# Performance work log

Measured on AMD Instinct MI355X. Metric: run time of the kernel, lower is better.

The kernel has to match this reference:

```python
import jax, jax.numpy as jnp
import numpy as np

LP, LQ, B, IN, HID = 256, 256, 32, 512, 512
H = 2 * HID          # internal hidden size (hidden_size * 2)
IN2 = 2 * IN         # Up/Uq feature dim after self-concat
IN4 = 4 * IN


def setup_inputs() -> dict:
    key = jax.random.key(0)
    ks = jax.random.split(key, 12)
    def w(k, shape, fan):
        return (jax.random.normal(k, shape, jnp.float32) / np.float32(np.sqrt(fan)))
    return {
        "up": jax.random.normal(ks[0], (LP, B, IN), jnp.float32),
        "uq": jax.random.normal(ks[1], (LQ, B, IN), jnp.float32),
        "v0": jax.random.normal(ks[2], (B, H), jnp.float32),    # torch.randn v
        "Vvec": jax.random.normal(ks[3], (B, H), jnp.float32),  # torch.randn V (squeezed)
        "Wp": w(ks[4], (H, IN2), IN2),
        "Wq": w(ks[5], (H, IN2), IN2),
        "Wv": w(ks[6], (H, H), H),
        "Wg": w(ks[7], (IN4, IN4), IN4),
        "W_ih": w(ks[8], (3 * H, IN2), IN2),
        "W_hh": w(ks[9], (3 * H, H), H),
        "b_ih": w(ks[10], (3 * H,), H),
        "b_hh": w(ks[11], (3 * H,), H),
    }


def reference(up, uq, v0, Vvec, Wp, Wq, Wv, Wg, W_ih, W_hh, b_ih, b_hh):
    in2 = 2 * up.shape[2]
    # mixer indices are arange -> Up/Uq are just feature self-concats
    Up = jnp.concatenate([up, up], axis=2)   # [lp, B, in2]
    Uq = jnp.concatenate([uq, uq], axis=2)   # [lq, B, in2]
    # hoist loop-invariant projections (original recomputes Wq(Uq) each step)
    WUp = jnp.einsum('pbi,hi->pbh', Up, Wp)  # [lp, B, H]
    WUq = jnp.einsum('qbi,hi->qbh', Uq, Wq)  # [lq, B, H]

    def gru_cell(x, h):
        gi = x @ W_ih.T + b_ih
        gh = h @ W_hh.T + b_hh
        i_r, i_z, i_n = jnp.split(gi, 3, axis=1)
        h_r, h_z, h_n = jnp.split(gh, 3, axis=1)
        r = jax.nn.sigmoid(i_r + h_r)
        z = jax.nn.sigmoid(i_z + h_z)
        n = jnp.tanh(i_n + r * h_n)
        return (1.0 - z) * n + z * h

    def step(v, xs):
        up_i, wup_i = xs                                   # [B,in2], [B,H]
        x = jnp.tanh(wup_i[None] + WUq + (v @ Wv.T)[None])  # [lq, B, H]
        s = jnp.einsum('qbh,bh->bq', x, Vvec)               # [B, lq]
        a = jax.nn.softmax(s, axis=1)
        c = jnp.einsum('bq,qbd->bd', a, Uq)                 # [B, in2]
        r = jnp.concatenate([up_i, c], axis=1)              # [B, in4]
        g = jax.nn.sigmoid(r @ Wg.T)
        c_ = (g * r)[:, in2:]                               # gated context half
        v_new = gru_cell(c_, v)
        return v_new, v_new

    _, vs = jax.lax.scan(step, v0, (Up, WUp))   # vs: [lp, B, H]
    # dropout in eval mode = identity
    return vs
```

## Files before the change

### kernel.cpp

```cpp
#include <hip/hip_runtime.h>


#define NB 32
#define WOFF 16384

__device__ __forceinline__ float fsig(float x) { return 1.0f / (1.0f + __expf(-x)); }
__device__ __forceinline__ float ftanh(float x) { return 1.0f - 2.0f / (1.0f + __expf(2.0f * x)); }

__device__ __forceinline__ float wred(float a) {
#pragma unroll
  for (int o = 32; o >= 1; o >>= 1) a += __shfl_xor(a, o, 64);
  return a;
}

__device__ __forceinline__ float cload(const float* p) {
  return __hip_atomic_load(p, __ATOMIC_RELAXED, __HIP_MEMORY_SCOPE_AGENT);
}
__device__ __forceinline__ void cstore(float* p, float v) {
  __hip_atomic_store(p, v, __ATOMIC_RELAXED, __HIP_MEMORY_SCOPE_AGENT);
}
__device__ __forceinline__ int cloadi(const int* p) {
  return __hip_atomic_load(p, __ATOMIC_RELAXED, __HIP_MEMORY_SCOPE_AGENT);
}

__device__ __forceinline__ void bgbar(int* sub, int* root, int bar) {
  __syncthreads();
  if (threadIdx.x == 0) {
    int old = __hip_atomic_fetch_add(sub, 1, __ATOMIC_RELAXED, __HIP_MEMORY_SCOPE_AGENT);
    if (old == 16 * bar - 1)
      __hip_atomic_fetch_add(root, 1, __ATOMIC_RELAXED, __HIP_MEMORY_SCOPE_AGENT);
    int tgt = 4 * bar, spins = 0;
    for (;;) {
      if (cloadi(root) >= tgt) break;
      __builtin_amdgcn_s_sleep(2);
      if (((++spins) & 255) == 0 &&
          __hip_atomic_load(root, __ATOMIC_ACQUIRE, __HIP_MEMORY_SCOPE_AGENT) >= tgt)
        break;
    }
  }
  __syncthreads();
}

__global__ __launch_bounds__(256) void k_init(
    const float* __restrict__ v0, const float* __restrict__ Wp,
    const float* __restrict__ Wg, float* __restrict__ wsbase,
    float* __restrict__ vbuf, float* __restrict__ Wpf, float* __restrict__ Wg2f) {
  int i = blockIdx.x * 256 + threadIdx.x;
  if (i < WOFF) ((int*)wsbase)[i] = 0;
  if (i < NB * 1024) vbuf[i] = v0[i];
  if (i < 1024 * 512) {
    int n = i >> 9, k = i & 511;
    Wpf[i] = Wp[(size_t)n * 1024 + k] + Wp[(size_t)n * 1024 + k + 512];
  }
  if (i < 1024 * 1024) {
    int j = i >> 10, kk = i & 1023;
    const float* wr = Wg + (size_t)(1024 + j) * 2048;
    Wg2f[i] = (kk < 512) ? (wr[kk] + wr[kk + 512]) : (wr[kk + 512] + wr[kk + 1024]);
  }
}

__global__ __launch_bounds__(256) void k_wuq(
    const float* __restrict__ A, const float* __restrict__ Wq, float* __restrict__ C) {
  __shared__ float As[16][65];
  __shared__ float Bs[16][65];
  int bm = blockIdx.x * 64, bn = blockIdx.y * 64;
  int t = threadIdx.x;
  int tx = t & 15, ty = t >> 4;
  float acc[4][4] = {};
  for (int k0 = 0; k0 < 512; k0 += 16) {
#pragma unroll
    for (int l = 0; l < 4; ++l) {
      int idx = t + l * 256;
      int row = idx >> 4, kk = idx & 15;
      As[kk][row] = A[(size_t)(bm + row) * 512 + k0 + kk];
      Bs[kk][row] = Wq[(size_t)(bn + row) * 1024 + k0 + kk] +
                    Wq[(size_t)(bn + row) * 1024 + k0 + kk + 512];
    }
    __syncthreads();
#pragma unroll
    for (int kk = 0; kk < 16; ++kk) {
      float a0[4], b0[4];
#pragma unroll
      for (int i = 0; i < 4; ++i) a0[i] = As[kk][ty * 4 + i];
#pragma unroll
      for (int j = 0; j < 4; ++j) b0[j] = Bs[kk][tx * 4 + j];
#pragma unroll
      for (int i = 0; i < 4; ++i)
#pragma unroll
        for (int j = 0; j < 4; ++j) acc[i][j] += a0[i] * b0[j];
    }
    __syncthreads();
  }
#pragma unroll
  for (int i = 0; i < 4; ++i)
#pragma unroll
    for (int j = 0; j < 4; ++j)
      C[(size_t)(bm + ty * 4 + i) * 1024 + bn + tx * 4 + j] = acc[i][j];
}

__global__ __launch_bounds__(512, 2) void k_loop(
    const float* __restrict__ up, const float* __restrict__ uq,
    const float* __restrict__ Vvec, const float* __restrict__ Wv,
    const float* __restrict__ W_hh, const float* __restrict__ b_hh,
    const float* __restrict__ W_ih, const float* __restrict__ b_ih,
    float* __restrict__ out, float* __restrict__ ws) {
  int* cbase = (int*)ws;

  float* vbuf  = ws + WOFF;
  float* tbuf  = ws + WOFF + 32768;
  float* ghbuf = ws + WOFF + 65536;
  float* sbuf  = ws + WOFF + 163840;
  float* chalf = ws + WOFF + 172032;
  float* cbuf  = ws + WOFF + 188416;
  float* Wpf   = ws + WOFF + 221184;
  float* Wg2f  = ws + WOFF + 745472;
  float* WUq   = ws + WOFF + 1794048;

  int bid = blockIdx.x;
  int tid = threadIdx.x, lane = tid & 63, wave = tid >> 6;

  __shared__ float smem[12288];

  int s = bid & 63, bg = bid >> 6, b0 = bg * 8;
  bool is_t = (s < 16);
  int b3 = b0 + (s >> 3), i0 = (s & 7) * 64;

  int* subc = cbase + (bg * 8 + (s >> 4)) * 64;
  int* rootc = cbase + (bg * 8 + 4) * 64;

  float vvreg[16];
#pragma unroll
  for (int i = 0; i < 16; ++i)
    vvreg[i] = Vvec[(size_t)(b0 + wave) * 1024 + lane + i * 64];

  int ho5 = tid >> 3, bb5 = tid & 7;
  int h5 = s * 16 + ho5, b5 = b0 + bb5;
  float vloc = 0.0f;
  if (tid < 128) vloc = cload(vbuf + (size_t)b5 * 1024 + h5);

  int bar = 0;

  for (int p = 0; p < 256; ++p) {
    {
      float tmp[16];
#pragma unroll
      for (int i = 0; i < 16; ++i)
        tmp[i] = cload(vbuf + (size_t)b0 * 1024 + tid + i * 512);
#pragma unroll
      for (int i = 0; i < 16; ++i) smem[tid + i * 512] = tmp[i];
      if (is_t) {
        float tu[8];
#pragma unroll
        for (int i = 0; i < 8; ++i)
          tu[i] = up[((size_t)p * NB + b0) * 512 + tid + i * 512];
#pragma unroll
        for (int i = 0; i < 8; ++i) smem[8192 + tid + i * 512] = tu[i];
      }
      __syncthreads();
      float vreg[8][16];
#pragma unroll
      for (int bb = 0; bb < 8; ++bb)
#pragma unroll
        for (int i = 0; i < 16; ++i)
          vreg[bb][i] = smem[bb * 1024 + lane + i * 64];
      int n0 = s * 64 + wave * 8;
      for (int rr = 0; rr < 8; ++rr) {
        int n = n0 + rr;
        float acc[8];
#pragma unroll
        for (int bb = 0; bb < 8; ++bb) acc[bb] = 0.0f;
        if (is_t) {
          const float* wr = Wv + (size_t)n * 1024;
#pragma unroll
          for (int i = 0; i < 16; ++i) {
            float w = wr[lane + i * 64];
#pragma unroll
            for (int bb = 0; bb < 8; ++bb) acc[bb] = fmaf(w, vreg[bb][i], acc[bb]);
          }
          const float* wp = Wpf + (size_t)n * 512;
#pragma unroll
          for (int i = 0; i < 8; ++i) {
            float w = wp[lane + i * 64];
#pragma unroll
            for (int bb = 0; bb < 8; ++bb)
              acc[bb] = fmaf(w, smem[8192 + bb * 512 + lane + i * 64], acc[bb]);
          }
#pragma unroll
          for (int bb = 0; bb < 8; ++bb) {
            float a = wred(acc[bb]);
            if (lane == 0) cstore(tbuf + (size_t)(b0 + bb) * 1024 + n, a);
          }
        } else {
          int m = n - 1024;
          const float* wr = W_hh + (size_t)m * 1024;
#pragma unroll
          for (int i = 0; i < 16; ++i) {
            float w = wr[lane + i * 64];
#pragma unroll
            for (int bb = 0; bb < 8; ++bb) acc[bb] = fmaf(w, vreg[bb][i], acc[bb]);
          }
          float bias = b_hh[m];
#pragma unroll
          for (int bb = 0; bb < 8; ++bb) {
            float a = wred(acc[bb]);
            if (lane == 0) cstore(ghbuf + (size_t)(b0 + bb) * 3072 + m, a + bias);
          }
        }
      }
    }
    ++bar; bgbar(subc, rootc, bar);

    {
      float tmp[16];
#pragma unroll
      for (int i = 0; i < 16; ++i)
        tmp[i] = cload(tbuf + (size_t)b0 * 1024 + tid + i * 512);
#pragma unroll
      for (int i = 0; i < 16; ++i) smem[tid + i * 512] = tmp[i];
      __syncthreads();
      float treg[16];
#pragma unroll
      for (int i = 0; i < 16; ++i) treg[i] = smem[wave * 1024 + lane + i * 64];
      int bq = b0 + wave;
      for (int qq = 0; qq < 4; ++qq) {
        int q = s * 4 + qq;
        const float* wu = WUq + ((size_t)q * NB + bq) * 1024;
        float a = 0.0f;
#pragma unroll
        for (int i = 0; i < 16; ++i)
          a += ftanh(treg[i] + __builtin_nontemporal_load(wu + lane + i * 64)) * vvreg[i];
        a = wred(a);
        if (lane == 0) cstore(sbuf + bq * 256 + q, a);
      }
    }
    ++bar; bgbar(subc, rootc, bar);

    {
      float* a_s  = smem;
      float* red  = smem + 256;
      float* part = smem + 512;
      int b = b3;
      float sv = -1e30f;
      if (tid < 256) sv = cload(sbuf + b * 256 + tid);
      float m = sv;
#pragma unroll
      for (int o = 32; o >= 1; o >>= 1) m = fmaxf(m, __shfl_xor(m, o, 64));
      if (lane == 0 && wave < 4) red[wave] = m;
      __syncthreads();
      float bm = fmaxf(fmaxf(red[0], red[1]), fmaxf(red[2], red[3]));
      __syncthreads();
      float e = 0.0f;
      if (tid < 256) e = __expf(sv - bm);
      float se = e;
#pragma unroll
      for (int o = 32; o >= 1; o >>= 1) se += __shfl_xor(se, o, 64);
      if (lane == 0 && wave < 4) red[wave] = se;
      __syncthreads();
      float tot = red[0] + red[1] + red[2] + red[3];
      if (tid < 256) a_s[tid] = e / tot;
      __syncthreads();
      float acc = 0.0f;
      for (int qq = 0; qq < 32; ++qq) {
        int q = wave * 32 + qq;
        acc += a_s[q] *
               __builtin_nontemporal_load(uq + ((size_t)q * NB + b) * 512 + i0 + lane);
      }
      part[wave * 64 + lane] = acc;
      __syncthreads();
      if (tid < 64) {
        float c = 0.0f;
#pragma unroll
        for (int w = 0; w < 8; ++w) c += part[w * 64 + tid];
        cstore(chalf + (size_t)b * 512 + i0 + tid, c);
      }
    }
    ++bar; bgbar(subc, rootc, bar);

    {
      float tc[8];
#pragma unroll
      for (int i = 0; i < 8; ++i)
        tc[i] = cload(chalf + (size_t)b0 * 512 + tid + i * 512);
#pragma unroll
      for (int i = 0; i < 8; ++i) smem[tid + i * 512] = tc[i];
      __syncthreads();
      float rreg[8][16];
#pragma unroll
      for (int bb = 0; bb < 8; ++bb) {
#pragma unroll
        for (int i = 0; i < 8; ++i)
          rreg[bb][i] = up[((size_t)p * NB + b0 + bb) * 512 + lane + i * 64];
#pragma unroll
        for (int i = 0; i < 8; ++i)
          rreg[bb][8 + i] = smem[bb * 512 + lane + i * 64];
      }
      int j0 = s * 16 + wave * 2;
      for (int rr = 0; rr < 2; ++rr) {
        int j = j0 + rr;
        const float* wr = Wg2f + (size_t)j * 1024;
        float acc[8];
#pragma unroll
        for (int bb = 0; bb < 8; ++bb) acc[bb] = 0.0f;
#pragma unroll
        for (int i = 0; i < 16; ++i) {
          float w = wr[lane + i * 64];
#pragma unroll
          for (int bb = 0; bb < 8; ++bb) acc[bb] = fmaf(w, rreg[bb][i], acc[bb]);
        }
#pragma unroll
        for (int bb = 0; bb < 8; ++bb) {
          float a = wred(acc[bb]);
          if (lane == 0) {
            float cv = smem[bb * 512 + (j & 511)];
            cstore(cbuf + (size_t)(b0 + bb) * 1024 + j, fsig(a) * cv);
          }
        }
      }
    }
    ++bar; bgbar(subc, rootc, bar);

    {
      float ghr = 0.0f, ghz = 0.0f, ghn = 0.0f;
      if (tid < 128) {
        const float* ghb = ghbuf + (size_t)b5 * 3072;
        ghr = cload(ghb + h5);
        ghz = cload(ghb + 1024 + h5);
        ghn = cload(ghb + 2048 + h5);
      }
      float tmp[16];
#pragma unroll
      for (int i = 0; i < 16; ++i)
        tmp[i] = cload(cbuf + (size_t)b0 * 1024 + tid + i * 512);
#pragma unroll
      for (int i = 0; i < 16; ++i) smem[tid + i * 512] = tmp[i];
      __syncthreads();
      float creg[8][16];
#pragma unroll
      for (int bb = 0; bb < 8; ++bb)
#pragma unroll
        for (int i = 0; i < 16; ++i)
          creg[bb][i] = smem[bb * 1024 + lane + i * 64];
      float* gi_s = smem + 8192;
      for (int k = 0; k < 6; ++k) {
        int idx = wave * 6 + k;
        int g = idx >> 4, ho = idx & 15;
        int r = g * 1024 + s * 16 + ho;
        const float* wr = W_ih + (size_t)r * 1024;
        float acc[8];
#pragma unroll
        for (int bb = 0; bb < 8; ++bb) acc[bb] = 0.0f;
#pragma unroll
        for (int i = 0; i < 16; ++i) {
          float w = wr[lane + i * 64];
#pragma unroll
          for (int bb = 0; bb < 8; ++bb) acc[bb] = fmaf(w, creg[bb][i], acc[bb]);
        }
        float bias = b_ih[r];
#pragma unroll
        for (int bb = 0; bb < 8; ++bb) {
          float a = wred(acc[bb]);
          if (lane == 0) gi_s[idx * 8 + bb] = a + bias;
        }
      }
      __syncthreads();
      if (tid < 128) {
        float gir = gi_s[(0 * 16 + ho5) * 8 + bb5];
        float giz = gi_s[(1 * 16 + ho5) * 8 + bb5];
        float gin = gi_s[(2 * 16 + ho5) * 8 + bb5];
        float rg = fsig(gir + ghr);
        float z  = fsig(giz + ghz);
        float nn = ftanh(gin + rg * ghn);
        float vn = (1.0f - z) * nn + z * vloc;
        vloc = vn;
        cstore(vbuf + (size_t)b5 * 1024 + h5, vn);
        __builtin_nontemporal_store(vn, out + ((size_t)p * NB + b5) * 1024 + h5);
      }
    }
    ++bar; bgbar(subc, rootc, bar);
  }
}

extern "C" void kernel_launch(void* const* d_in, const int* in_sizes, int n_in,
                              void* d_out, int out_size, void* d_ws, size_t ws_size,
                              hipStream_t stream) {
  const float* up = (const float*)d_in[0];
  const float* uq = (const float*)d_in[1];
  const float* v0 = (const float*)d_in[2];
  const float* Vvec = (const float*)d_in[3];
  const float* Wp = (const float*)d_in[4];
  const float* Wq = (const float*)d_in[5];
  const float* Wv = (const float*)d_in[6];
  const float* Wg = (const float*)d_in[7];
  const float* W_ih = (const float*)d_in[8];
  const float* W_hh = (const float*)d_in[9];
  const float* b_ih = (const float*)d_in[10];
  const float* b_hh = (const float*)d_in[11];
  float* out = (float*)d_out;
  float* ws = (float*)d_ws;

  float* vbuf = ws + WOFF;
  float* Wpf  = ws + WOFF + 221184;
  float* Wg2f = ws + WOFF + 745472;
  float* WUq  = ws + WOFF + 1794048;

  k_init<<<4096, 256, 0, stream>>>(v0, Wp, Wg, ws, vbuf, Wpf, Wg2f);
  k_wuq<<<dim3(128, 16), 256, 0, stream>>>(uq, Wq, WUq);
  k_loop<<<256, 512, 0, stream>>>(up, uq, Vvec, Wv, W_hh, b_hh, W_ih, b_ih, out, ws);
}
```

Before: 32.34 ms.

## Prefetch per-phase weights and inputs into registers before grid barriers

Loads for the next phase (WUq rows, uq context rows, Wg rows, the first two W_ih rows and the gh gate values) are issued into registers before each grid-wide barrier instead of after it. Their memory latency can then overlap the barrier wait in this persistent, barrier-heavy recurrent kernel. The prefetch loops are fully unrolled and the data stays in registers. The cost is higher VGPR pressure across barriers, which could cause spills or lower occupancy.

```diff
diff --git a/kernel.cpp b/kernel.cpp
--- a/kernel.cpp
+++ b/kernel.cpp
@@ -208,6 +208,16 @@
         }
       }
     }
+    float wuq_pf[4][16];
+    {
+      int bq = b0 + wave;
+#pragma unroll
+      for (int qq = 0; qq < 4; ++qq) {
+        const float* wu = WUq + ((size_t)(s * 4 + qq) * NB + bq) * 1024;
+#pragma unroll
+        for (int i = 0; i < 16; ++i) wuq_pf[qq][i] = wu[lane + i * 64];
+      }
+    }
     ++bar; bgbar(subc, rootc, bar);
 
     {
@@ -222,17 +232,21 @@
 #pragma unroll
       for (int i = 0; i < 16; ++i) treg[i] = smem[wave * 1024 + lane + i * 64];
       int bq = b0 + wave;
+#pragma unroll
       for (int qq = 0; qq < 4; ++qq) {
         int q = s * 4 + qq;
-        const float* wu = WUq + ((size_t)q * NB + bq) * 1024;
         float a = 0.0f;
 #pragma unroll
         for (int i = 0; i < 16; ++i)
-          a += ftanh(treg[i] + __builtin_nontemporal_load(wu + lane + i * 64)) * vvreg[i];
+          a += ftanh(treg[i] + wuq_pf[qq][i]) * vvreg[i];
         a = wred(a);
         if (lane == 0) cstore(sbuf + bq * 256 + q, a);
       }
     }
+    float uq_pf[32];
+#pragma unroll
+    for (int qq = 0; qq < 32; ++qq)
+      uq_pf[qq] = uq[((size_t)(wave * 32 + qq) * NB + b3) * 512 + i0 + lane];
     ++bar; bgbar(subc, rootc, bar);
 
     {
@@ -260,11 +274,9 @@
       if (tid < 256) a_s[tid] = e / tot;
       __syncthreads();
       float acc = 0.0f;
-      for (int qq = 0; qq < 32; ++qq) {
-        int q = wave * 32 + qq;
-        acc += a_s[q] *
-               __builtin_nontemporal_load(uq + ((size_t)q * NB + b) * 512 + i0 + lane);
-      }
+#pragma unroll
+      for (int qq = 0; qq < 32; ++qq)
+        acc += a_s[wave * 32 + qq] * uq_pf[qq];
       part[wave * 64 + lane] = acc;
       __syncthreads();
       if (tid < 64) {
@@ -274,6 +286,16 @@
         cstore(chalf + (size_t)b * 512 + i0 + tid, c);
       }
     }
+    float wg_pf[2][16];
+    {
+      int j0 = s * 16 + wave * 2;
+#pragma unroll
+      for (int rr = 0; rr < 2; ++rr) {
+        const float* wr = Wg2f + (size_t)(j0 + rr) * 1024;
+#pragma unroll
+        for (int i = 0; i < 16; ++i) wg_pf[rr][i] = wr[lane + i * 64];
+      }
+    }
     ++bar; bgbar(subc, rootc, bar);
 
     {
@@ -295,15 +317,15 @@
           rreg[bb][8 + i] = smem[bb * 512 + lane + i * 64];
       }
       int j0 = s * 16 + wave * 2;
+#pragma unroll
       for (int rr = 0; rr < 2; ++rr) {
         int j = j0 + rr;
-        const float* wr = Wg2f + (size_t)j * 1024;
         float acc[8];
 #pragma unroll
         for (int bb = 0; bb < 8; ++bb) acc[bb] = 0.0f;
 #pragma unroll
         for (int i = 0; i < 16; ++i) {
-          float w = wr[lane + i * 64];
+          float w = wg_pf[rr][i];
 #pragma unroll
           for (int bb = 0; bb < 8; ++bb) acc[bb] = fmaf(w, rreg[bb][i], acc[bb]);
         }
@@ -317,16 +339,25 @@
         }
       }
     }
+    float wih_pf[2][16];
+#pragma unroll
+    for (int k = 0; k < 2; ++k) {
+      int idx = wave * 6 + k;
+      int r = (idx >> 4) * 1024 + s * 16 + (idx & 15);
+      const float* wr = W_ih + (size_t)r * 1024;
+#pragma unroll
+      for (int i = 0; i < 16; ++i) wih_pf[k][i] = wr[lane + i * 64];
+    }
+    float ghr = 0.0f, ghz = 0.0f, ghn = 0.0f;
+    if (tid < 128) {
+      const float* ghb = ghbuf + (size_t)b5 * 3072;
+      ghr = cload(ghb + h5);
+      ghz = cload(ghb + 1024 + h5);
+      ghn = cload(ghb + 2048 + h5);
+    }
     ++bar; bgbar(subc, rootc, bar);
 
     {
-      float ghr = 0.0f, ghz = 0.0f, ghn = 0.0f;
-      if (tid < 128) {
-        const float* ghb = ghbuf + (size_t)b5 * 3072;
-        ghr = cload(ghb + h5);
-        ghz = cload(ghb + 1024 + h5);
-        ghn = cload(ghb + 2048 + h5);
-      }
       float tmp[16];
 #pragma unroll
       for (int i = 0; i < 16; ++i)
@@ -351,7 +382,7 @@
         for (int bb = 0; bb < 8; ++bb) acc[bb] = 0.0f;
 #pragma unroll
         for (int i = 0; i < 16; ++i) {
-          float w = wr[lane + i * 64];
+          float w = (k < 2) ? wih_pf[k][i] : wr[lane + i * 64];
 #pragma unroll
           for (int bb = 0; bb < 8; ++bb) acc[bb] = fmaf(w, creg[bb][i], acc[bb]);
         }
```

New measurement: 37.91 ms. 1.17x slower.
